# Optimization experiments

Hardware: AMD Instinct MI355X
Metric: run time of the kernel (lower is better)

Reference implementation:

```python
import jax, jax.numpy as jnp
import numpy as np

EPS = 1e-5

def setup_inputs() -> dict:
    key = jax.random.key(0)
    kx, kw = jax.random.split(key)
    x = jax.random.normal(kx, (4, 2048, 4096), dtype=jnp.float32)
    W = jax.random.normal(kw, (4096, 4096), dtype=jnp.float32) * 0.02
    return {"x": x, "W": W}

def reference(x, W):
    # scale = mean absolute weight
    scale = jnp.mean(jnp.abs(W))
    Wn = W / (scale + EPS)
    # straight-through ternary rounding: forward = round(Wn), grad = identity
    Wq = Wn + jax.lax.stop_gradient(jnp.round(Wn) - Wn)
    # y = x @ Wq^T, then rescale by mean(|W|)
    y = jnp.einsum('bsi,oi->bso', x, Wq)
    return y * scale
```

## Files before the change

### kernel.cpp

```cpp
#include <hip/hip_runtime.h>


#define K_DIM 4096
#define N_DIM 4096
#define NKT   64

typedef __bf16 bf16x8 __attribute__((ext_vector_type(8)));
typedef float floatx4 __attribute__((ext_vector_type(4)));

__device__ __forceinline__ unsigned short f32_to_bf16(float f) {
    unsigned int u = __float_as_uint(f);
    u += 0x7fffu + ((u >> 16) & 1u);
    return (unsigned short)(u >> 16);
}

__global__ void reduce_abs_p1(const float4* __restrict__ W, double* __restrict__ partials, int n4) {
    int tid = blockIdx.x * blockDim.x + threadIdx.x;
    int stride = gridDim.x * blockDim.x;
    float s = 0.f;
    for (int i = tid; i < n4; i += stride) {
        float4 v = W[i];
        s += fabsf(v.x) + fabsf(v.y) + fabsf(v.z) + fabsf(v.w);
    }
    double d = (double)s;
#pragma unroll
    for (int o = 32; o > 0; o >>= 1) d += __shfl_down(d, o, 64);
    __shared__ double lds[4];
    if ((threadIdx.x & 63) == 0) lds[threadIdx.x >> 6] = d;
    __syncthreads();
    if (threadIdx.x == 0)
        partials[blockIdx.x] = lds[0] + lds[1] + lds[2] + lds[3];
}

__global__ void reduce_abs_p2(const double* __restrict__ partials, double* __restrict__ out) {
    double d = 0.0;
#pragma unroll
    for (int i = 0; i < 4; ++i) d += partials[threadIdx.x + i * 256];
#pragma unroll
    for (int o = 32; o > 0; o >>= 1) d += __shfl_down(d, o, 64);
    __shared__ double lds[4];
    if ((threadIdx.x & 63) == 0) lds[threadIdx.x >> 6] = d;
    __syncthreads();
    if (threadIdx.x == 0) *out = lds[0] + lds[1] + lds[2] + lds[3];
}

__global__ void prep(const float4* __restrict__ W, const float4* __restrict__ X,
                     const double* __restrict__ sum,
                     ushort4* __restrict__ Wq, ushort4* __restrict__ Xb,
                     int nW4, int nX4, double inv_cnt) {
    float scale = (float)(*sum * inv_cnt);
    float d = scale + 1e-5f;
    int tid = blockIdx.x * blockDim.x + threadIdx.x;
    int stride = gridDim.x * blockDim.x;
    for (int i = tid; i < nW4; i += stride) {
        float4 v = W[i];
        ushort4 q;
        q.x = f32_to_bf16(rintf(v.x / d));
        q.y = f32_to_bf16(rintf(v.y / d));
        q.z = f32_to_bf16(rintf(v.z / d));
        q.w = f32_to_bf16(rintf(v.w / d));
        Wq[i] = q;
    }
    for (int i = tid; i < nX4; i += stride) {
        float4 v = X[i];
        ushort4 q;
        q.x = f32_to_bf16(v.x);
        q.y = f32_to_bf16(v.y);
        q.z = f32_to_bf16(v.z);
        q.w = f32_to_bf16(v.w);
        Xb[i] = q;
    }
}

__global__ __launch_bounds__(512, 2) void gemm_bt(
    const unsigned short* __restrict__ A, const unsigned short* __restrict__ B,
    float* __restrict__ C, const double* __restrict__ sum, double inv_cnt) {

    __shared__ __attribute__((aligned(16))) unsigned short As[2][2][128 * 64];
    __shared__ __attribute__((aligned(16))) unsigned short Bs[2][2][128 * 64];

    const int tid  = threadIdx.x;
    const int w    = tid >> 6;
    const int lane = tid & 63;
    const int wm   = w >> 2;
    const int wn   = w & 3;

    const int bid = blockIdx.y * gridDim.x + blockIdx.x;
    const int swz = (bid & 7) * 64 + (bid >> 3);
    const size_t m0 = (size_t)(swz >> 4) * 256;
    const size_t n0 = (size_t)(swz & 15) * 256;

    const int srow   = lane >> 3;
    const int schunk = (lane & 7) ^ srow;
    const unsigned short* pA = A + (m0 + (size_t)(w * 8 + srow)) * K_DIM + schunk * 8;
    const unsigned short* pB = B + (n0 + (size_t)(w * 8 + srow)) * K_DIM + schunk * 8;

    const int fm    = lane & 15;
    const int q     = lane >> 4;
    const int cs0   = (q ^ (fm & 7)) * 8;
    const int cs1   = ((4 + q) ^ (fm & 7)) * 8;
    const int abase = fm * 64;
    const int bh    = wn >> 1;
    const int bbase = (wn & 1) * 4096 + fm * 64;

    floatx4 acc[8][4] = {};
    bf16x8 a0[2][4];
    bf16x8 a1[2][4];
    bf16x8 b0v[2][2];
    bf16x8 b1v[2][2];

#define STAGE_A(bb, h, kt) do {                                                            \
        __builtin_amdgcn_global_load_lds(                                                  \
            (const __attribute__((address_space(1))) void*)(pA + ((h) * 128 + 0) * K_DIM + (kt) * 64), \
            (__attribute__((address_space(3))) void*)&As[bb][h][w * 512 + 0], 16, 0, 0);   \
        __builtin_amdgcn_global_load_lds(                                                  \
            (const __attribute__((address_space(1))) void*)(pA + ((h) * 128 + 64) * K_DIM + (kt) * 64), \
            (__attribute__((address_space(3))) void*)&As[bb][h][w * 512 + 4096], 16, 0, 0); \
    } while (0)

#define STAGE_B(bb, h, kt) do {                                                            \
        __builtin_amdgcn_global_load_lds(                                                  \
            (const __attribute__((address_space(1))) void*)(pB + ((h) * 128 + 0) * K_DIM + (kt) * 64), \
            (__attribute__((address_space(3))) void*)&Bs[bb][h][w * 512 + 0], 16, 0, 0);   \
        __builtin_amdgcn_global_load_lds(                                                  \
            (const __attribute__((address_space(1))) void*)(pB + ((h) * 128 + 64) * K_DIM + (kt) * 64), \
            (__attribute__((address_space(3))) void*)&Bs[bb][h][w * 512 + 4096], 16, 0, 0); \
    } while (0)

#define READ_A_HALF(dst, b, mh) do {                                                       \
        _Pragma("unroll")                                                                  \
        for (int t = 0; t < 4; ++t) {                                                      \
            dst[0][t] = *(const bf16x8*)&As[b][wm][((mh) * 4 + t) * 1024 + abase + cs0];   \
            dst[1][t] = *(const bf16x8*)&As[b][wm][((mh) * 4 + t) * 1024 + abase + cs1];   \
        }                                                                                  \
    } while (0)

#define READ_B_HALF(dst, b, nh) do {                                                       \
        _Pragma("unroll")                                                                  \
        for (int u = 0; u < 2; ++u) {                                                      \
            dst[0][u] = *(const bf16x8*)&Bs[b][bh][bbase + ((nh) * 2 + u) * 1024 + cs0];   \
            dst[1][u] = *(const bf16x8*)&Bs[b][bh][bbase + ((nh) * 2 + u) * 1024 + cs1];   \
        }                                                                                  \
    } while (0)

#define MFMA16(mh, nh, Af, Bf) do {                                                        \
        _Pragma("unroll")                                                                  \
        for (int t = 0; t < 4; ++t)                                                        \
            _Pragma("unroll")                                                              \
            for (int u = 0; u < 2; ++u) {                                                  \
                acc[(mh) * 4 + t][(nh) * 2 + u] = __builtin_amdgcn_mfma_f32_16x16x32_bf16( \
                    Af[0][t], Bf[0][u], acc[(mh) * 4 + t][(nh) * 2 + u], 0, 0, 0);         \
                acc[(mh) * 4 + t][(nh) * 2 + u] = __builtin_amdgcn_mfma_f32_16x16x32_bf16( \
                    Af[1][t], Bf[1][u], acc[(mh) * 4 + t][(nh) * 2 + u], 0, 0, 0);         \
            }                                                                              \
    } while (0)

#define KTILE(b, j, DOA, DOB, PF, VM1S, VM2S) do {                                         \
                             \
        if (DOA) STAGE_A((b) ^ 1, 0, (j) + 1);                                             \
        READ_B_HALF(b1v, b, 1);                                                            \
        __builtin_amdgcn_s_setprio(1);                                                     \
        MFMA16(0, 0, a0, b0v);                                                             \
        __builtin_amdgcn_s_setprio(0);                                                     \
        asm volatile("s_waitcnt lgkmcnt(0)" ::: "memory");                                 \
        __builtin_amdgcn_s_barrier();                                                      \
                              \
        if (DOA) STAGE_A((b) ^ 1, 1, (j) + 1);                                             \
        READ_A_HALF(a1, b, 1);                                                             \
        __builtin_amdgcn_s_setprio(1);                                                     \
        MFMA16(0, 1, a0, b1v);                                                             \
        __builtin_amdgcn_s_setprio(0);                                                     \
        asm volatile(VM1S ::: "memory");                                                   \
        __builtin_amdgcn_s_barrier();                                                      \
                        \
        if (DOB) STAGE_B(b, 0, (j) + 2);                                                   \
        __builtin_amdgcn_s_setprio(1);                                                     \
        MFMA16(1, 0, a1, b0v);                                                             \
        __builtin_amdgcn_s_setprio(0);                                                     \
        if (PF) READ_B_HALF(b0v, (b) ^ 1, 0);                                              \
        asm volatile(VM2S ::: "memory");                                                   \
        __builtin_amdgcn_s_barrier();                                                      \
                        \
        if (DOB) STAGE_B(b, 1, (j) + 2);                                                   \
        if (PF) READ_A_HALF(a0, (b) ^ 1, 0);                                               \
        __builtin_amdgcn_s_setprio(1);                                                     \
        MFMA16(1, 1, a1, b1v);                                                             \
        __builtin_amdgcn_s_setprio(0);                                                     \
        asm volatile("s_waitcnt lgkmcnt(0)" ::: "memory");                                 \
        __builtin_amdgcn_s_barrier();                                                      \
    } while (0)

    STAGE_B(0, 0, 0); STAGE_B(0, 1, 0);
    STAGE_A(0, 0, 0); STAGE_A(0, 1, 0);
    STAGE_B(1, 0, 1); STAGE_B(1, 1, 1);
    asm volatile("s_waitcnt vmcnt(4)" ::: "memory");
    __builtin_amdgcn_s_barrier();
    READ_A_HALF(a0, 0, 0);
    READ_B_HALF(b0v, 0, 0);

    for (int j = 0; j < NKT - 2; j += 2) {
        KTILE(0, j,     1, (j < NKT - 2), 1, "s_waitcnt vmcnt(4)", "s_waitcnt vmcnt(2)");
        KTILE(1, j + 1, 1, (j + 1 < NKT - 2), 1, "s_waitcnt vmcnt(4)", "s_waitcnt vmcnt(2)");
    }
    KTILE(0, NKT - 2, 1, 0, 1, "s_waitcnt vmcnt(4)", "s_waitcnt vmcnt(0)");
    KTILE(1, NKT - 1, 0, 0, 0, "", "");

#undef KTILE
#undef MFMA16
#undef READ_B_HALF
#undef READ_A_HALF
#undef STAGE_B
#undef STAGE_A

    const float scale = (float)(*sum * inv_cnt);
    const size_t m0c = m0 + (size_t)wm * 128;
    const size_t n0c = n0 + (size_t)wn * 64;
#pragma unroll
    for (int mf = 0; mf < 8; ++mf) {
#pragma unroll
        for (int nf = 0; nf < 4; ++nf) {
            float* cp = C + (m0c + mf * 16 + q * 4) * N_DIM + n0c + nf * 16 + fm;
#pragma unroll
            for (int r = 0; r < 4; ++r)
                cp[(size_t)r * N_DIM] = acc[mf][nf][r] * scale;
        }
    }
}

extern "C" void kernel_launch(void* const* d_in, const int* in_sizes, int n_in,
                              void* d_out, int out_size, void* d_ws, size_t ws_size,
                              hipStream_t stream) {
    const float* x = (const float*)d_in[0];
    const float* W = (const float*)d_in[1];
    float* y = (float*)d_out;

    const int nW = in_sizes[1];
    const int M  = in_sizes[0] / K_DIM;

    double* d_sum = (double*)d_ws;
    double* d_partials = (double*)((char*)d_ws + 16);
    unsigned short* xb = (unsigned short*)((char*)d_ws + 16 + 1024 * sizeof(double));
    unsigned short* wq = xb + (size_t)M * K_DIM;
    const double inv_cnt = 1.0 / (double)nW;

    reduce_abs_p1<<<1024, 256, 0, stream>>>((const float4*)W, d_partials, nW / 4);
    reduce_abs_p2<<<1, 256, 0, stream>>>(d_partials, d_sum);
    prep<<<2048, 256, 0, stream>>>((const float4*)W, (const float4*)x, d_sum,
                                   (ushort4*)wq, (ushort4*)xb,
                                   nW / 4, in_sizes[0] / 4, inv_cnt);

    dim3 grid(N_DIM / 256, M / 256);
    gemm_bt<<<grid, 512, 0, stream>>>(xb, wq, y, d_sum, inv_cnt);
}
```

Baseline: 588.6 us.

## Fold final abs-sum reduction into prep and reorder GEMM MFMA/load schedule

Removes the single-block second reduction kernel: every prep block now re-reduces the 1024 partials itself, and block 0 writes the sum for the GEMM epilogue. This saves one kernel launch and its serialization, at the cost of redundant small reads in each block. The GEMM main loop is re-sequenced in several ways. It uses ping-pong B register sets (Be/Bo) so B prefetch can overlap the MFMA quadrants. It changes the quadrant order and splits the MFMA inner loop by k-substep. It replaces the lgkmcnt waits with extra barriers around each MFMA block. The extra barriers and the changed wait placement could add sync stalls or break the LDS read/write ordering.

```diff
diff --git a/kernel.cpp b/kernel.cpp
--- a/kernel.cpp
+++ b/kernel.cpp
@@ -32,23 +32,23 @@
         partials[blockIdx.x] = lds[0] + lds[1] + lds[2] + lds[3];
 }
 
-__global__ void reduce_abs_p2(const double* __restrict__ partials, double* __restrict__ out) {
-    double d = 0.0;
-#pragma unroll
-    for (int i = 0; i < 4; ++i) d += partials[threadIdx.x + i * 256];
-#pragma unroll
-    for (int o = 32; o > 0; o >>= 1) d += __shfl_down(d, o, 64);
-    __shared__ double lds[4];
-    if ((threadIdx.x & 63) == 0) lds[threadIdx.x >> 6] = d;
-    __syncthreads();
-    if (threadIdx.x == 0) *out = lds[0] + lds[1] + lds[2] + lds[3];
-}
-
 __global__ void prep(const float4* __restrict__ W, const float4* __restrict__ X,
-                     const double* __restrict__ sum,
+                     const double* __restrict__ partials, double* __restrict__ sum_out,
                      ushort4* __restrict__ Wq, ushort4* __restrict__ Xb,
                      int nW4, int nX4, double inv_cnt) {
-    float scale = (float)(*sum * inv_cnt);
+    __shared__ double lds[4];
+    double dsum;
+    {
+        int t = threadIdx.x;
+        double d = partials[t] + partials[t + 256] + partials[t + 512] + partials[t + 768];
+#pragma unroll
+        for (int o = 32; o > 0; o >>= 1) d += __shfl_down(d, o, 64);
+        if ((t & 63) == 0) lds[t >> 6] = d;
+        __syncthreads();
+        dsum = lds[0] + lds[1] + lds[2] + lds[3];
+        if (blockIdx.x == 0 && t == 0) *sum_out = dsum;
+    }
+    float scale = (float)(dsum * inv_cnt);
     float d = scale + 1e-5f;
     int tid = blockIdx.x * blockDim.x + threadIdx.x;
     int stride = gridDim.x * blockDim.x;
@@ -106,8 +106,8 @@
     floatx4 acc[8][4] = {};
     bf16x8 a0[2][4];
     bf16x8 a1[2][4];
-    bf16x8 b0v[2][2];
-    bf16x8 b1v[2][2];
+    bf16x8 Be[2][2];
+    bf16x8 Bo[2][2];
 
 #define STAGE_A(bb, h, kt) do {                                                            \
         __builtin_amdgcn_global_load_lds(                                                  \
@@ -145,65 +145,66 @@
 
 #define MFMA16(mh, nh, Af, Bf) do {                                                        \
         _Pragma("unroll")                                                                  \
-        for (int t = 0; t < 4; ++t)                                                        \
+        for (int ks = 0; ks < 2; ++ks)                                                     \
             _Pragma("unroll")                                                              \
-            for (int u = 0; u < 2; ++u) {                                                  \
-                acc[(mh) * 4 + t][(nh) * 2 + u] = __builtin_amdgcn_mfma_f32_16x16x32_bf16( \
-                    Af[0][t], Bf[0][u], acc[(mh) * 4 + t][(nh) * 2 + u], 0, 0, 0);         \
-                acc[(mh) * 4 + t][(nh) * 2 + u] = __builtin_amdgcn_mfma_f32_16x16x32_bf16( \
-                    Af[1][t], Bf[1][u], acc[(mh) * 4 + t][(nh) * 2 + u], 0, 0, 0);         \
-            }                                                                              \
-    } while (0)
-
-#define KTILE(b, j, DOA, DOB, PF, VM1S, VM2S) do {                                         \
-                             \
+            for (int t = 0; t < 4; ++t)                                                    \
+                _Pragma("unroll")                                                          \
+                for (int u = 0; u < 2; ++u)                                                \
+                    acc[(mh) * 4 + t][(nh) * 2 + u] = __builtin_amdgcn_mfma_f32_16x16x32_bf16( \
+                        Af[ks][t], Bf[ks][u], acc[(mh) * 4 + t][(nh) * 2 + u], 0, 0, 0);   \
+    } while (0)
+
+#define KTILE(b, j, P, Q, DOA, DOB, PFB, PFA, VM1S, VM2S) do {                             \
+                                 \
+        READ_B_HALF(Q, b, 1);                                                              \
         if (DOA) STAGE_A((b) ^ 1, 0, (j) + 1);                                             \
-        READ_B_HALF(b1v, b, 1);                                                            \
-        __builtin_amdgcn_s_setprio(1);                                                     \
-        MFMA16(0, 0, a0, b0v);                                                             \
-        __builtin_amdgcn_s_setprio(0);                                                     \
-        asm volatile("s_waitcnt lgkmcnt(0)" ::: "memory");                                 \
+        __builtin_amdgcn_s_barrier();                                                      \
+        __builtin_amdgcn_s_setprio(1);                                                     \
+        MFMA16(0, 0, a0, P);                                                               \
+        __builtin_amdgcn_s_setprio(0);                                                     \
+        __builtin_amdgcn_s_barrier();                                                      \
+                                    \
+        READ_A_HALF(a1, b, 1);                                                             \
+        if (DOA) STAGE_A((b) ^ 1, 1, (j) + 1);                                             \
+        __builtin_amdgcn_s_barrier();                                                      \
+        __builtin_amdgcn_s_setprio(1);                                                     \
+        MFMA16(0, 1, a0, Q);                                                               \
+        __builtin_amdgcn_s_setprio(0);                                                     \
+        asm volatile(VM1S ::: "memory");                                                   \
+        __builtin_amdgcn_s_barrier();                                                      \
+                          \
+        if (DOB) STAGE_B(b, 0, (j) + 2);                                                   \
+        __builtin_amdgcn_s_barrier();                                                      \
+        __builtin_amdgcn_s_setprio(1);                                                     \
+        MFMA16(1, 1, a1, Q);                                                               \
+        __builtin_amdgcn_s_setprio(0);                                                     \
+        if (PFB) READ_B_HALF(Q, (b) ^ 1, 0);                                               \
+        asm volatile(VM2S ::: "memory");                                                   \
         __builtin_amdgcn_s_barrier();                                                      \
                               \
-        if (DOA) STAGE_A((b) ^ 1, 1, (j) + 1);                                             \
-        READ_A_HALF(a1, b, 1);                                                             \
-        __builtin_amdgcn_s_setprio(1);                                                     \
-        MFMA16(0, 1, a0, b1v);                                                             \
-        __builtin_amdgcn_s_setprio(0);                                                     \
-        asm volatile(VM1S ::: "memory");                                                   \
-        __builtin_amdgcn_s_barrier();                                                      \
-                        \
-        if (DOB) STAGE_B(b, 0, (j) + 2);                                                   \
-        __builtin_amdgcn_s_setprio(1);                                                     \
-        MFMA16(1, 0, a1, b0v);                                                             \
-        __builtin_amdgcn_s_setprio(0);                                                     \
-        if (PF) READ_B_HALF(b0v, (b) ^ 1, 0);                                              \
-        asm volatile(VM2S ::: "memory");                                                   \
-        __builtin_amdgcn_s_barrier();                                                      \
-                        \
+        if (PFA) READ_A_HALF(a0, (b) ^ 1, 0);                                              \
         if (DOB) STAGE_B(b, 1, (j) + 2);                                                   \
-        if (PF) READ_A_HALF(a0, (b) ^ 1, 0);                                               \
-        __builtin_amdgcn_s_setprio(1);                                                     \
-        MFMA16(1, 1, a1, b1v);                                                             \
-        __builtin_amdgcn_s_setprio(0);                                                     \
-        asm volatile("s_waitcnt lgkmcnt(0)" ::: "memory");                                 \
-        __builtin_amdgcn_s_barrier();                                                      \
-    } while (0)
-
+        __builtin_amdgcn_s_barrier();                                                      \
+        __builtin_amdgcn_s_setprio(1);                                                     \
+        MFMA16(1, 0, a1, P);                                                               \
+        __builtin_amdgcn_s_setprio(0);                                                     \
+        __builtin_amdgcn_s_barrier();                                                      \
+    } while (0)
+
+    STAGE_A(0, 0, 0); STAGE_A(0, 1, 0);
     STAGE_B(0, 0, 0); STAGE_B(0, 1, 0);
-    STAGE_A(0, 0, 0); STAGE_A(0, 1, 0);
     STAGE_B(1, 0, 1); STAGE_B(1, 1, 1);
     asm volatile("s_waitcnt vmcnt(4)" ::: "memory");
     __builtin_amdgcn_s_barrier();
     READ_A_HALF(a0, 0, 0);
-    READ_B_HALF(b0v, 0, 0);
+    READ_B_HALF(Be, 0, 0);
 
     for (int j = 0; j < NKT - 2; j += 2) {
-        KTILE(0, j,     1, (j < NKT - 2), 1, "s_waitcnt vmcnt(4)", "s_waitcnt vmcnt(2)");
-        KTILE(1, j + 1, 1, (j + 1 < NKT - 2), 1, "s_waitcnt vmcnt(4)", "s_waitcnt vmcnt(2)");
-    }
-    KTILE(0, NKT - 2, 1, 0, 1, "s_waitcnt vmcnt(4)", "s_waitcnt vmcnt(0)");
-    KTILE(1, NKT - 1, 0, 0, 0, "", "");
+        KTILE(0, j,     Be, Bo, 1, 1, 1, 1, "s_waitcnt vmcnt(4)", "s_waitcnt vmcnt(2)");
+        KTILE(1, j + 1, Bo, Be, 1, 1, 1, 1, "s_waitcnt vmcnt(4)", "s_waitcnt vmcnt(2)");
+    }
+    KTILE(0, NKT - 2, Be, Bo, 1, 0, 1, 1, "s_waitcnt vmcnt(4)", "s_waitcnt vmcnt(0)");
+    KTILE(1, NKT - 1, Bo, Be, 0, 0, 0, 0, "", "");
 
 #undef KTILE
 #undef MFMA16
@@ -244,8 +245,7 @@
     const double inv_cnt = 1.0 / (double)nW;
 
     reduce_abs_p1<<<1024, 256, 0, stream>>>((const float4*)W, d_partials, nW / 4);
-    reduce_abs_p2<<<1, 256, 0, stream>>>(d_partials, d_sum);
-    prep<<<2048, 256, 0, stream>>>((const float4*)W, (const float4*)x, d_sum,
+    prep<<<2048, 256, 0, stream>>>((const float4*)W, (const float4*)x, d_partials, d_sum,
                                    (ushort4*)wq, (ushort4*)xb,
                                    nW / 4, in_sizes[0] / 4, inv_cnt);
 
```

Measured after the change: 578.6 us. No clear change (-1.7%).
